# Performance work log

Hardware: AMD Instinct MI355X
Metric: run time of the kernel (lower is better)

## Reference

```python
import jax, jax.numpy as jnp
import numpy as np
from jax.scipy.linalg import expm

LATENT, HIDDEN, N_PARTS, K = 128, 2048, 128, 2048
OMEGA_DIM, TRANZ_DIM = 9 * N_PARTS, 3 * N_PARTS


def setup_inputs() -> dict:
    key = jax.random.key(0)
    ks = jax.random.split(key, 10)

    def w(k, out_d, in_d):
        # eqx.nn.Linear-style scale ~ 1/sqrt(fan_in)
        return jax.random.normal(k, (out_d, in_d), dtype=jnp.float32) / np.sqrt(in_d)

    return {
        "x_init": jax.random.normal(ks[0], (LATENT, K), dtype=jnp.float32),
        "Wo0": w(ks[1], HIDDEN, LATENT),
        "Wo1": w(ks[2], HIDDEN, HIDDEN),
        "Wo2": w(ks[3], HIDDEN, HIDDEN),
        "Wo3": w(ks[4], OMEGA_DIM, HIDDEN),
        "Wt0": w(ks[5], HIDDEN, LATENT),
        "Wt1": w(ks[6], HIDDEN, HIDDEN),
        "Wt2": w(ks[7], HIDDEN, HIDDEN),
        "Wt3": w(ks[8], TRANZ_DIM, HIDDEN),
    }


def _mlp(weights, x):
    # bias-free MLP, relu on all but last layer; x is (d_in, K)
    for i, W in enumerate(weights):
        x = W @ x
        if i + 1 < len(weights):
            x = jax.nn.relu(x)
    return x


def reference(x_init, Wo0, Wo1, Wo2, Wo3, Wt0, Wt1, Wt2, Wt3):
    omega = _mlp([Wo0, Wo1, Wo2, Wo3], x_init)            # (9n, K)
    n = omega.shape[0] // 9
    k = omega.shape[1]
    # exp_omega 2D branch: vmap over columns, each column -> (n,3,3) expm batch
    mats = omega.T.reshape(k * n, 3, 3)
    R = jax.vmap(expm)(mats).reshape(k, 9 * n)            # (K, 9n)
    rotations = R.T                                        # (9n, K)
    translations = _mlp([Wt0, Wt1, Wt2, Wt3], x_init)     # (3n, K)
    # form_transformations (2D branch): stack translation as a 4th row -> (12n, K)
    rot_r = rotations.reshape(n, 3, 3, k)
    tr_r = translations.reshape(n, 1, 3, k)
    transf = jnp.concatenate([rot_r, tr_r], axis=1).reshape(-1, k)  # (12n, K)
    return (omega, transf, rotations, translations)
```

## Files before the change

kernel.cpp:

```cpp
#include <hip/hip_runtime.h>
#include <stdint.h>


typedef short bf16x8 __attribute__((ext_vector_type(8)));
typedef float f32x4 __attribute__((ext_vector_type(4)));

__device__ __forceinline__ unsigned short f2bf(float f) {
  unsigned int x = __float_as_uint(f);
  unsigned int r = (x + 0x7fffu + ((x >> 16) & 1u)) >> 16;
  return (unsigned short)r;
}

__device__ __forceinline__ void gld_lds16(const void* g, void* l) {
  __builtin_amdgcn_global_load_lds(
      (__attribute__((address_space(1))) void*)(g),
      (__attribute__((address_space(3))) void*)(l),
      16, 0, 0);
}

__device__ __forceinline__ unsigned lds_addr(const void* p) {
  return (unsigned)(uintptr_t)(__attribute__((address_space(3))) const void*)p;
}

__device__ __forceinline__ bf16x8 ds_read128(unsigned a) {
  bf16x8 r;
  asm volatile("ds_read_b128 %0, %1" : "=v"(r) : "v"(a));
  return r;
}

#define ASM_BAR asm volatile("s_barrier" ::: "memory")
#define LGKM0   asm volatile("s_waitcnt lgkmcnt(0)" ::: "memory")
#define VMCNT0  asm volatile("s_waitcnt vmcnt(0)" ::: "memory")
#define SCHED0  __builtin_amdgcn_sched_barrier(0)

__global__ void prep_k(const float* __restrict__ x,
                       const float* __restrict__ wo0, const float* __restrict__ wo1,
                       const float* __restrict__ wo2, const float* __restrict__ wo3,
                       const float* __restrict__ wt0, const float* __restrict__ wt1,
                       const float* __restrict__ wt2, const float* __restrict__ wt3,
                       unsigned short* __restrict__ dst, unsigned short* __restrict__ xt) {
  __shared__ float tile[32][33];
  const int b = blockIdx.x;
  const int tid = threadIdx.x;
  if (b >= 9984) {
    const int r = b - 9984;
    const int bx = r & 63, by = r >> 6;
    const int tx = tid & 31, ty = tid >> 5;
#pragma unroll
    for (int i = 0; i < 32; i += 8)
      tile[ty + i][tx] = x[(size_t)(by * 32 + ty + i) * 2048 + bx * 32 + tx];
    __syncthreads();
#pragma unroll
    for (int i = 0; i < 32; i += 8)
      xt[(size_t)(bx * 32 + ty + i) * 128 + by * 32 + tx] = f2bf(tile[tx][ty + i]);
    return;
  }
  int idx = (b * 256 + tid) * 8;
  if (idx >= 20447232) return;
  const float* src;
  int off;
  if (idx < 8650752) {
    if (idx < 262144)       { src = wo0; off = idx; }
    else if (idx < 4456448) { src = wo1; off = idx - 262144; }
    else                    { src = wo2; off = idx - 4456448; }
  } else {
    if (idx < 11010048)      { src = wo3; off = idx - 8650752; }
    else if (idx < 11272192) { src = wt0; off = idx - 11010048; }
    else if (idx < 15466496) { src = wt1; off = idx - 11272192; }
    else if (idx < 19660800) { src = wt2; off = idx - 15466496; }
    else                     { src = wt3; off = idx - 19660800; }
  }
  float4 a = *(const float4*)(src + off);
  float4 c = *(const float4*)(src + off + 4);
  uint4 o;
  o.x = (unsigned)f2bf(a.x) | ((unsigned)f2bf(a.y) << 16);
  o.y = (unsigned)f2bf(a.z) | ((unsigned)f2bf(a.w) << 16);
  o.z = (unsigned)f2bf(c.x) | ((unsigned)f2bf(c.y) << 16);
  o.w = (unsigned)f2bf(c.z) | ((unsigned)f2bf(c.w) << 16);
  *(uint4*)(dst + idx) = o;
}

template <int SWZ>
__global__ __launch_bounds__(256, 2) void gemm_tn(
    const unsigned short* __restrict__ A0, const unsigned short* __restrict__ B0,
    unsigned short* __restrict__ C0, int n0tiles, int ldc0,
    const unsigned short* __restrict__ A1, const unsigned short* __restrict__ B1,
    unsigned short* __restrict__ C1, int ldc1, int K) {
  __shared__ alignas(16) unsigned short Asl[128 * 128];
  __shared__ alignas(16) unsigned short Bsl[128 * 128];

  int mt, yt;
  if (SWZ) {
    int id = blockIdx.x;
    int xcd = id & 7, s = id >> 3;
    mt = ((xcd & 1) << 3) + (s & 7);
    yt = ((xcd >> 1) << 3) + (s >> 3);
  } else {
    mt = blockIdx.x;
    yt = blockIdx.y;
  }

  const unsigned short* A;
  const unsigned short* B;
  unsigned short* C;
  int ldc;
  if (yt < n0tiles) { A = A0; B = B0; C = C0; ldc = ldc0; }
  else { A = A1; B = B1; C = C1; ldc = ldc1; yt -= n0tiles; }

  const unsigned short* Ab = A + (size_t)mt * 128 * K;
  const unsigned short* Bb = B + (size_t)yt * 128 * K;

  const int tid = threadIdx.x;
  const int wave = tid >> 6, lane = tid & 63;
  const int mw = (wave >> 1) * 64, nw = (wave & 1) * 64;
  const int l16 = lane & 15, quad = lane >> 4;

  f32x4 acc[4][4] = {};

  for (int k0 = 0; k0 < K; k0 += 128) {
#pragma unroll
    for (int i = 0; i < 8; ++i) {
      int c = i * 256 + tid;
      int row = c >> 4;
      int l = (c & 15) ^ (row & 15);
      gld_lds16(Ab + (size_t)row * K + k0 + l * 8, &Asl[c * 8]);
      gld_lds16(Bb + (size_t)row * K + k0 + l * 8, &Bsl[c * 8]);
    }
    __syncthreads();

#pragma unroll
    for (int h = 0; h < 4; ++h) {
      bf16x8 af[4], bfr[4];
#pragma unroll
      for (int t = 0; t < 4; ++t) {
        int row = mw + t * 16 + l16;
        int p = (h * 4 + quad) ^ (row & 15);
        af[t] = *(const bf16x8*)&Asl[row * 128 + p * 8];
      }
#pragma unroll
      for (int t = 0; t < 4; ++t) {
        int row = nw + t * 16 + l16;
        int p = (h * 4 + quad) ^ (row & 15);
        bfr[t] = *(const bf16x8*)&Bsl[row * 128 + p * 8];
      }
#pragma unroll
      for (int tm = 0; tm < 4; ++tm)
#pragma unroll
        for (int tn = 0; tn < 4; ++tn)
          acc[tm][tn] = __builtin_amdgcn_mfma_f32_16x16x32_bf16(af[tm], bfr[tn], acc[tm][tn], 0, 0, 0);
    }
    __syncthreads();
  }

  const int mbase = mt * 128 + mw;
  const int nbase = yt * 128 + nw;
#pragma unroll
  for (int tm = 0; tm < 4; ++tm) {
#pragma unroll
    for (int tn = 0; tn < 4; ++tn) {
      int col = nbase + tn * 16 + l16;
      int row0 = mbase + tm * 16 + quad * 4;
#pragma unroll
      for (int r = 0; r < 4; ++r) {
        float v = fmaxf(acc[tm][tn][r], 0.0f);
        C[(size_t)(row0 + r) * ldc + col] = f2bf(v);
      }
    }
  }
}

__global__ __launch_bounds__(256, 2) void gemm_db128(
    const unsigned short* __restrict__ A0, const unsigned short* __restrict__ B0,
    unsigned short* __restrict__ C0,
    const unsigned short* __restrict__ A1, const unsigned short* __restrict__ B1,
    unsigned short* __restrict__ C1, int K) {
  __shared__ alignas(16) unsigned short SM[2 * 16384];

  const int id = blockIdx.x;
  const int xcd = id & 7, s = id >> 3;
  const int mt = s & 15;
  const int ntt = xcd * 4 + (s >> 4);

  const unsigned short* A;
  const unsigned short* B;
  unsigned short* C;
  int ntl;
  if (ntt < 16) { A = A0; B = B0; C = C0; ntl = ntt; }
  else          { A = A1; B = B1; C = C1; ntl = ntt - 16; }

  const unsigned short* Ab = A + (size_t)mt * 128 * K;
  const unsigned short* Bb = B + (size_t)ntl * 128 * K;

  const int tid = threadIdx.x;
  const int wave = tid >> 6, lane = tid & 63;
  const int mw = (wave >> 1) * 64, nw = (wave & 1) * 64;
  const int l16 = lane & 15, quad = lane >> 4;

  const unsigned short* gA[4];
  const unsigned short* gB[4];
  int dAo[4], dBo[4];
#pragma unroll
  for (int i = 0; i < 4; ++i) {
    int c = i * 256 + tid;
    int row = c >> 3, pc = c & 7, l = pc ^ (row & 7);
    gA[i] = Ab + (size_t)row * K + l * 8;
    dAo[i] = c * 8;
    gB[i] = Bb + (size_t)row * K + l * 8;
    dBo[i] = 8192 + c * 8;
  }

  unsigned aoff[2][4], boff[2][4];
#pragma unroll
  for (int ph = 0; ph < 2; ++ph)
#pragma unroll
    for (int i = 0; i < 4; ++i) {
      int ra = mw + i * 16 + l16;
      aoff[ph][i] = (unsigned)(ra * 128 + (((ph * 4 + quad) ^ (ra & 7)) * 16));
      int rb = nw + i * 16 + l16;
      boff[ph][i] = (unsigned)(16384 + rb * 128 + (((ph * 4 + quad) ^ (rb & 7)) * 16));
    }
  const unsigned Au = lds_addr(SM);

  f32x4 acc[4][4] = {};
  const int NT = K >> 6;

  auto STAGE = [&](int slot, int k1) {
    const int so = slot * 16384;
#pragma unroll
    for (int i = 0; i < 4; ++i) gld_lds16(gA[i] + k1, SM + so + dAo[i]);
#pragma unroll
    for (int i = 0; i < 4; ++i) gld_lds16(gB[i] + k1, SM + so + dBo[i]);
  };

  STAGE(0, 0);
  VMCNT0;
  ASM_BAR;

  int cur = 0;
  for (int t = 0; t < NT; ++t) {
    int k1 = (t + 1) << 6;
    if (k1 > K - 64) k1 = K - 64;
    STAGE(cur ^ 1, k1);

    const unsigned base = Au + cur * 32768;
    bf16x8 a0[4], b0[4], a1[4], b1[4];
#pragma unroll
    for (int i = 0; i < 4; ++i) a0[i] = ds_read128(base + aoff[0][i]);
#pragma unroll
    for (int i = 0; i < 4; ++i) b0[i] = ds_read128(base + boff[0][i]);
#pragma unroll
    for (int i = 0; i < 4; ++i) a1[i] = ds_read128(base + aoff[1][i]);
#pragma unroll
    for (int i = 0; i < 4; ++i) b1[i] = ds_read128(base + boff[1][i]);
    LGKM0;
    SCHED0;
    __builtin_amdgcn_s_setprio(1);
#pragma unroll
    for (int tm = 0; tm < 4; ++tm)
#pragma unroll
      for (int tn = 0; tn < 4; ++tn)
        acc[tm][tn] = __builtin_amdgcn_mfma_f32_16x16x32_bf16(a0[tm], b0[tn], acc[tm][tn], 0, 0, 0);
#pragma unroll
    for (int tm = 0; tm < 4; ++tm)
#pragma unroll
      for (int tn = 0; tn < 4; ++tn)
        acc[tm][tn] = __builtin_amdgcn_mfma_f32_16x16x32_bf16(a1[tm], b1[tn], acc[tm][tn], 0, 0, 0);
    __builtin_amdgcn_s_setprio(0);
    SCHED0;

    VMCNT0;
    ASM_BAR;
    cur ^= 1;
  }

  const int mbase = mt * 128 + mw;
  const int nbase = ntl * 128 + nw;
#pragma unroll
  for (int tm = 0; tm < 4; ++tm) {
#pragma unroll
    for (int tn = 0; tn < 4; ++tn) {
      int col = nbase + tn * 16 + l16;
      int row0 = mbase + tm * 16 + quad * 4;
#pragma unroll
      for (int r = 0; r < 4; ++r) {
        float v = fmaxf(acc[tm][tn][r], 0.0f);
        C[(size_t)(row0 + r) * 2048 + col] = f2bf(v);
      }
    }
  }
}

__device__ __forceinline__ void mm3(const float* a, const float* b, float* c) {
#pragma unroll
  for (int r = 0; r < 3; ++r)
#pragma unroll
    for (int cc = 0; cc < 3; ++cc)
      c[r * 3 + cc] = a[r * 3 + 0] * b[0 + cc] + a[r * 3 + 1] * b[3 + cc] + a[r * 3 + 2] * b[6 + cc];
}

__device__ __forceinline__ void expm3(const float* a, float* E) {
  float n1 = 0.f;
#pragma unroll
  for (int c = 0; c < 3; ++c) {
    float s = fabsf(a[c]) + fabsf(a[3 + c]) + fabsf(a[6 + c]);
    n1 = fmaxf(n1, s);
  }
  int s = 0;
  if (n1 > 0.25f) {
    s = (int)ceilf(log2f(n1 * 4.0f));
    if (s < 0) s = 0;
  }
  const float scl = exp2f((float)(-s));
  float As[9];
#pragma unroll
  for (int i = 0; i < 9; ++i) As[i] = a[i] * scl;
  float T[9] = {1, 0, 0, 0, 1, 0, 0, 0, 1};
#pragma unroll
  for (int i = 0; i < 9; ++i) E[i] = T[i];
#pragma unroll
  for (int t = 1; t <= 12; ++t) {
    float Tn[9];
    mm3(T, As, Tn);
    const float inv = 1.0f / (float)t;
#pragma unroll
    for (int i = 0; i < 9; ++i) { T[i] = Tn[i] * inv; E[i] += T[i]; }
  }
  for (int q = 0; q < s; ++q) {
    float Tn[9];
    mm3(E, E, Tn);
#pragma unroll
    for (int i = 0; i < 9; ++i) E[i] = Tn[i];
  }
}

__global__ __launch_bounds__(256, 1) void gemm_l3u(
    const unsigned short* __restrict__ Ho, const unsigned short* __restrict__ W9,
    const unsigned short* __restrict__ Ht, const unsigned short* __restrict__ W3,
    float* __restrict__ out) {
  __shared__ alignas(16) unsigned short SM[40960];
  float* Cl = (float*)SM;

  const int mt = blockIdx.x;
  const int yt = blockIdx.y;
  const int tid = threadIdx.x;
  const int wave = tid >> 6, lane = tid & 63;
  const int wm = wave >> 1, wn = wave & 1;
  const int l16 = lane & 15, quad = lane >> 4;
  const int mbase = mt * 64;

  float* omega  = out;
  float* transf = out + (size_t)1152 * 2048;
  float* rot    = out + (size_t)(1152 + 1536) * 2048;
  float* transl = out + (size_t)(1152 + 1536 + 1152) * 2048;

  const unsigned short* Ao  = Ho + (size_t)mbase * 2048;
  const unsigned short* At  = Ht + (size_t)mbase * 2048;
  const unsigned short* W9p = W9 + (size_t)yt * 144 * 2048;
  const unsigned short* W3p = W3 + (size_t)yt * 48 * 2048;

  const unsigned short* gAo[2];
  const unsigned short* gAt[2];
  int dA[2];
#pragma unroll
  for (int i = 0; i < 2; ++i) {
    int c = i * 256 + tid, row = c >> 3, pc = c & 7, l = pc ^ (row & 7);
    gAo[i] = Ao + (size_t)row * 2048 + l * 8;
    gAt[i] = At + (size_t)row * 2048 + l * 8;
    dA[i] = c * 8;
  }
  const unsigned short* gB[6];
  int dB[6];
#pragma unroll
  for (int i = 0; i < 6; ++i) {
    int c = i * 256 + tid, row = c >> 3, pc = c & 7, l = pc ^ (row & 7);
    gB[i] = (row < 144 ? W9p + (size_t)row * 2048
                       : W3p + (size_t)(row - 144) * 2048) + l * 8;
    dB[i] = c * 8;
  }

  auto STAGE = [&](int s, int k1) {
    const int ao = s * 4096, at = 8192 + s * 4096, bo = 16384 + s * 12288;
#pragma unroll
    for (int i = 0; i < 2; ++i) gld_lds16(gAo[i] + k1, SM + ao + dA[i]);
#pragma unroll
    for (int i = 0; i < 2; ++i) gld_lds16(gAt[i] + k1, SM + at + dA[i]);
#pragma unroll
    for (int i = 0; i < 6; ++i) gld_lds16(gB[i] + k1, SM + bo + dB[i]);
  };

  unsigned aoff[2][2], boff[2][6];
#pragma unroll
  for (int ph = 0; ph < 2; ++ph) {
#pragma unroll
    for (int tm = 0; tm < 2; ++tm) {
      int ra = wm * 32 + tm * 16 + l16;
      aoff[ph][tm] = (unsigned)(ra * 128 + (((ph * 4 + quad) ^ (ra & 7)) * 16));
    }
#pragma unroll
    for (int tb = 0; tb < 6; ++tb) {
      int rb = (wn * 6 + tb) * 16 + l16;
      boff[ph][tb] = (unsigned)(rb * 128 + (((ph * 4 + quad) ^ (rb & 7)) * 16));
    }
  }
  const unsigned Au = lds_addr(SM);

  f32x4 acc[2][6] = {};

  STAGE(0, 0);
  VMCNT0;
  ASM_BAR;

  int cur = 0;
  for (int t = 0; t < 32; ++t) {
    int k1 = (t + 1) << 6;
    if (k1 > 2048 - 64) k1 = 2048 - 64;
    STAGE(cur ^ 1, k1);

    const unsigned aoB = Au + cur * 8192;
    const unsigned atB = Au + 16384 + cur * 8192;
    const unsigned bB  = Au + 32768 + cur * 24576;
    bf16x8 a0o[2], a1o[2], a0t[2], a1t[2], b0[6], b1[6];
#pragma unroll
    for (int i = 0; i < 2; ++i) {
      a0o[i] = ds_read128(aoB + aoff[0][i]);
      a1o[i] = ds_read128(aoB + aoff[1][i]);
    }
    if (wn) {
#pragma unroll
      for (int i = 0; i < 2; ++i) {
        a0t[i] = ds_read128(atB + aoff[0][i]);
        a1t[i] = ds_read128(atB + aoff[1][i]);
      }
    }
#pragma unroll
    for (int i = 0; i < 6; ++i) {
      b0[i] = ds_read128(bB + boff[0][i]);
      b1[i] = ds_read128(bB + boff[1][i]);
    }
    LGKM0;
    SCHED0;
    if (!wn) {
#pragma unroll
      for (int i = 0; i < 2; ++i) { a0t[i] = a0o[i]; a1t[i] = a1o[i]; }
    }
    __builtin_amdgcn_s_setprio(1);
#pragma unroll
    for (int tm = 0; tm < 2; ++tm)
#pragma unroll
      for (int tb = 0; tb < 6; ++tb)
        acc[tm][tb] = __builtin_amdgcn_mfma_f32_16x16x32_bf16(
            tb >= 3 ? a0t[tm] : a0o[tm], b0[tb], acc[tm][tb], 0, 0, 0);
#pragma unroll
    for (int tm = 0; tm < 2; ++tm)
#pragma unroll
      for (int tb = 0; tb < 6; ++tb)
        acc[tm][tb] = __builtin_amdgcn_mfma_f32_16x16x32_bf16(
            tb >= 3 ? a1t[tm] : a1o[tm], b1[tb], acc[tm][tb], 0, 0, 0);
    __builtin_amdgcn_s_setprio(0);
    SCHED0;

    VMCNT0;
    ASM_BAR;
    cur ^= 1;
  }

#pragma unroll
  for (int tm = 0; tm < 2; ++tm) {
#pragma unroll
    for (int tb = 0; tb < 6; ++tb) {
      int st = wn * 6 + tb;
      int s0 = wm * 32 + tm * 16 + quad * 4;
      if (st < 9) {
        int d = st * 16 + l16;
        *(f32x4*)&Cl[d * 68 + s0] = acc[tm][tb];
      } else {
        int n = yt * 48 + (st - 9) * 16 + l16;
        int row0 = mbase + s0;
        int j = n / 3, c2 = n % 3;
        *(f32x4*)&transl[(size_t)n * 2048 + row0] = acc[tm][tb];
        *(f32x4*)&transf[(size_t)(12 * j + 9 + c2) * 2048 + row0] = acc[tm][tb];
      }
    }
  }
  __syncthreads();

  const int jbase = yt * 16;
  const int k = mbase + lane;
#pragma unroll 1
  for (int pp = 0; pp < 4; ++pp) {
    int pl = wave * 4 + pp;
    int j = jbase + pl;
    float a[9];
#pragma unroll
    for (int i = 0; i < 9; ++i) a[i] = Cl[(pl * 9 + i) * 68 + lane];
#pragma unroll
    for (int i = 0; i < 9; ++i) omega[(size_t)(9 * j + i) * 2048 + k] = a[i];
    float E[9];
    expm3(a, E);
#pragma unroll
    for (int i = 0; i < 9; ++i) {
      rot[(size_t)(9 * j + i) * 2048 + k] = E[i];
      transf[(size_t)(12 * j + i) * 2048 + k] = E[i];
    }
  }
}

extern "C" void kernel_launch(void* const* d_in, const int* in_sizes, int n_in,
                              void* d_out, int out_size, void* d_ws, size_t ws_size,
                              hipStream_t stream) {
  const float* x   = (const float*)d_in[0];
  const float* Wo0 = (const float*)d_in[1];
  const float* Wo1 = (const float*)d_in[2];
  const float* Wo2 = (const float*)d_in[3];
  const float* Wo3 = (const float*)d_in[4];
  const float* Wt0 = (const float*)d_in[5];
  const float* Wt1 = (const float*)d_in[6];
  const float* Wt2 = (const float*)d_in[7];
  const float* Wt3 = (const float*)d_in[8];

  unsigned short* wb   = (unsigned short*)d_ws;
  unsigned short* wo0b = wb + 0;
  unsigned short* wo1b = wb + 262144;
  unsigned short* wo2b = wb + 4456448;
  unsigned short* wo3b = wb + 8650752;
  unsigned short* wt0b = wb + 11010048;
  unsigned short* wt1b = wb + 11272192;
  unsigned short* wt2b = wb + 15466496;
  unsigned short* wt3b = wb + 19660800;
  unsigned short* Xt   = wb + 20447232;
  unsigned short* HoA  = Xt + 262144;
  unsigned short* HoB  = HoA + 4194304;
  unsigned short* HtA  = HoB + 4194304;
  unsigned short* HtB  = HtA + 4194304;

  prep_k<<<10240, 256, 0, stream>>>(x, Wo0, Wo1, Wo2, Wo3, Wt0, Wt1, Wt2, Wt3, wb, Xt);

  gemm_tn<1><<<512, 256, 0, stream>>>(Xt, wo0b, HoA, 16, 2048,
                                      Xt, wt0b, HtA, 2048, 128);
  gemm_db128<<<512, 256, 0, stream>>>(HoA, wo1b, HoB, HtA, wt1b, HtB, 2048);
  gemm_db128<<<512, 256, 0, stream>>>(HoB, wo2b, HoA, HtB, wt2b, HtA, 2048);
  gemm_l3u<<<dim3(32, 8), 256, 0, stream>>>(HoA, wo3b, HtA, wt3b, (float*)d_out);
}
```

Before: 237.4 us.

## Split final layer GEMM from expm into separate kernels with finer tiling

The fused last-layer GEMM plus expm kernel (256 blocks of 64x192 tiles, one block per CU) is replaced by a plain GEMM with 64x96 tiles over 512 blocks, two allowed per CU, followed by a separate elementwise expm kernel that reads omega back from global memory. The intent is to fill the GPU better and overlap loads, and to spread the expm work across more threads. The cost is an extra launch, a global round trip for omega, and the loss of the A-tile sharing between the omega and translation chains.

```diff
diff --git a/kernel.cpp b/kernel.cpp
--- a/kernel.cpp
+++ b/kernel.cpp
@@ -290,121 +290,74 @@
   }
 }
 
-__device__ __forceinline__ void mm3(const float* a, const float* b, float* c) {
-#pragma unroll
-  for (int r = 0; r < 3; ++r)
-#pragma unroll
-    for (int cc = 0; cc < 3; ++cc)
-      c[r * 3 + cc] = a[r * 3 + 0] * b[0 + cc] + a[r * 3 + 1] * b[3 + cc] + a[r * 3 + 2] * b[6 + cc];
-}
-
-__device__ __forceinline__ void expm3(const float* a, float* E) {
-  float n1 = 0.f;
-#pragma unroll
-  for (int c = 0; c < 3; ++c) {
-    float s = fabsf(a[c]) + fabsf(a[3 + c]) + fabsf(a[6 + c]);
-    n1 = fmaxf(n1, s);
-  }
-  int s = 0;
-  if (n1 > 0.25f) {
-    s = (int)ceilf(log2f(n1 * 4.0f));
-    if (s < 0) s = 0;
-  }
-  const float scl = exp2f((float)(-s));
-  float As[9];
-#pragma unroll
-  for (int i = 0; i < 9; ++i) As[i] = a[i] * scl;
-  float T[9] = {1, 0, 0, 0, 1, 0, 0, 0, 1};
-#pragma unroll
-  for (int i = 0; i < 9; ++i) E[i] = T[i];
-#pragma unroll
-  for (int t = 1; t <= 12; ++t) {
-    float Tn[9];
-    mm3(T, As, Tn);
-    const float inv = 1.0f / (float)t;
-#pragma unroll
-    for (int i = 0; i < 9; ++i) { T[i] = Tn[i] * inv; E[i] += T[i]; }
-  }
-  for (int q = 0; q < s; ++q) {
-    float Tn[9];
-    mm3(E, E, Tn);
-#pragma unroll
-    for (int i = 0; i < 9; ++i) E[i] = Tn[i];
-  }
-}
-
-__global__ __launch_bounds__(256, 1) void gemm_l3u(
+__global__ __launch_bounds__(256, 2) void gemm_l3s(
     const unsigned short* __restrict__ Ho, const unsigned short* __restrict__ W9,
     const unsigned short* __restrict__ Ht, const unsigned short* __restrict__ W3,
     float* __restrict__ out) {
-  __shared__ alignas(16) unsigned short SM[40960];
-  float* Cl = (float*)SM;
-
-  const int mt = blockIdx.x;
-  const int yt = blockIdx.y;
+  __shared__ alignas(16) unsigned short SM[2 * 4096 + 2 * 6144];
+
+  const int id = blockIdx.x;
+  const int mt = id & 31;
+  const int nt = id >> 5;
+
+  float* omega  = out;
+  float* transf = out + (size_t)1152 * 2048;
+  float* transl = out + (size_t)(1152 + 1536 + 1152) * 2048;
+
+  const int chain1 = (nt >= 12);
+  const unsigned short* A;
+  const unsigned short* B;
+  if (!chain1) { A = Ho; B = W9 + (size_t)nt * 96 * 2048; }
+  else         { A = Ht; B = W3 + (size_t)(nt - 12) * 96 * 2048; }
+  const unsigned short* Ab = A + (size_t)mt * 64 * 2048;
+
   const int tid = threadIdx.x;
   const int wave = tid >> 6, lane = tid & 63;
-  const int wm = wave >> 1, wn = wave & 1;
+  const int mw = (wave >> 1) * 32, nw = (wave & 1) * 48;
   const int l16 = lane & 15, quad = lane >> 4;
-  const int mbase = mt * 64;
-
-  float* omega  = out;
-  float* transf = out + (size_t)1152 * 2048;
-  float* rot    = out + (size_t)(1152 + 1536) * 2048;
-  float* transl = out + (size_t)(1152 + 1536 + 1152) * 2048;
-
-  const unsigned short* Ao  = Ho + (size_t)mbase * 2048;
-  const unsigned short* At  = Ht + (size_t)mbase * 2048;
-  const unsigned short* W9p = W9 + (size_t)yt * 144 * 2048;
-  const unsigned short* W3p = W3 + (size_t)yt * 48 * 2048;
-
-  const unsigned short* gAo[2];
-  const unsigned short* gAt[2];
+
+  const unsigned short* gA[2];
   int dA[2];
 #pragma unroll
   for (int i = 0; i < 2; ++i) {
     int c = i * 256 + tid, row = c >> 3, pc = c & 7, l = pc ^ (row & 7);
-    gAo[i] = Ao + (size_t)row * 2048 + l * 8;
-    gAt[i] = At + (size_t)row * 2048 + l * 8;
+    gA[i] = Ab + (size_t)row * 2048 + l * 8;
     dA[i] = c * 8;
   }
-  const unsigned short* gB[6];
-  int dB[6];
-#pragma unroll
-  for (int i = 0; i < 6; ++i) {
+  const unsigned short* gB[3];
+  int dB[3];
+#pragma unroll
+  for (int i = 0; i < 3; ++i) {
     int c = i * 256 + tid, row = c >> 3, pc = c & 7, l = pc ^ (row & 7);
-    gB[i] = (row < 144 ? W9p + (size_t)row * 2048
-                       : W3p + (size_t)(row - 144) * 2048) + l * 8;
+    gB[i] = B + (size_t)row * 2048 + l * 8;
     dB[i] = c * 8;
   }
 
   auto STAGE = [&](int s, int k1) {
-    const int ao = s * 4096, at = 8192 + s * 4096, bo = 16384 + s * 12288;
-#pragma unroll
-    for (int i = 0; i < 2; ++i) gld_lds16(gAo[i] + k1, SM + ao + dA[i]);
-#pragma unroll
-    for (int i = 0; i < 2; ++i) gld_lds16(gAt[i] + k1, SM + at + dA[i]);
-#pragma unroll
-    for (int i = 0; i < 6; ++i) gld_lds16(gB[i] + k1, SM + bo + dB[i]);
+    const int sa = s * 4096, sb = 8192 + s * 6144;
+#pragma unroll
+    for (int i = 0; i < 2; ++i) gld_lds16(gA[i] + k1, SM + sa + dA[i]);
+#pragma unroll
+    for (int i = 0; i < 3; ++i) gld_lds16(gB[i] + k1, SM + sb + dB[i]);
   };
 
-  unsigned aoff[2][2], boff[2][6];
+  unsigned aoff[2][2], boff[2][3];
 #pragma unroll
   for (int ph = 0; ph < 2; ++ph) {
 #pragma unroll
     for (int tm = 0; tm < 2; ++tm) {
-      int ra = wm * 32 + tm * 16 + l16;
+      int ra = mw + tm * 16 + l16;
       aoff[ph][tm] = (unsigned)(ra * 128 + (((ph * 4 + quad) ^ (ra & 7)) * 16));
     }
 #pragma unroll
-    for (int tb = 0; tb < 6; ++tb) {
-      int rb = (wn * 6 + tb) * 16 + l16;
-      boff[ph][tb] = (unsigned)(rb * 128 + (((ph * 4 + quad) ^ (rb & 7)) * 16));
+    for (int tn = 0; tn < 3; ++tn) {
+      int rb = nw + tn * 16 + l16;
+      boff[ph][tn] = (unsigned)(rb * 128 + (((ph * 4 + quad) ^ (rb & 7)) * 16));
     }
   }
   const unsigned Au = lds_addr(SM);
 
-  f32x4 acc[2][6] = {};
+  f32x4 acc[2][3] = {};
 
   STAGE(0, 0);
   VMCNT0;
@@ -416,46 +369,30 @@
     if (k1 > 2048 - 64) k1 = 2048 - 64;
     STAGE(cur ^ 1, k1);
 
-    const unsigned aoB = Au + cur * 8192;
-    const unsigned atB = Au + 16384 + cur * 8192;
-    const unsigned bB  = Au + 32768 + cur * 24576;
-    bf16x8 a0o[2], a1o[2], a0t[2], a1t[2], b0[6], b1[6];
-#pragma unroll
-    for (int i = 0; i < 2; ++i) {
-      a0o[i] = ds_read128(aoB + aoff[0][i]);
-      a1o[i] = ds_read128(aoB + aoff[1][i]);
-    }
-    if (wn) {
-#pragma unroll
-      for (int i = 0; i < 2; ++i) {
-        a0t[i] = ds_read128(atB + aoff[0][i]);
-        a1t[i] = ds_read128(atB + aoff[1][i]);
-      }
-    }
-#pragma unroll
-    for (int i = 0; i < 6; ++i) {
-      b0[i] = ds_read128(bB + boff[0][i]);
-      b1[i] = ds_read128(bB + boff[1][i]);
-    }
+    const unsigned aB = Au + cur * 8192;
+    const unsigned bB = Au + 16384 + cur * 12288;
+    bf16x8 a0[2], b0[3], a1[2], b1[3];
+#pragma unroll
+    for (int i = 0; i < 2; ++i) a0[i] = ds_read128(aB + aoff[0][i]);
+#pragma unroll
+    for (int i = 0; i < 3; ++i) b0[i] = ds_read128(bB + boff[0][i]);
+#pragma unroll
+    for (int i = 0; i < 2; ++i) a1[i] = ds_read128(aB + aoff[1][i]);
+#pragma unroll
+    for (int i = 0; i < 3; ++i) b1[i] = ds_read128(bB + boff[1][i]);
     LGKM0;
     SCHED0;
-    if (!wn) {
-#pragma unroll
-      for (int i = 0; i < 2; ++i) { a0t[i] = a0o[i]; a1t[i] = a1o[i]; }
-    }
     __builtin_amdgcn_s_setprio(1);
 #pragma unroll
     for (int tm = 0; tm < 2; ++tm)
 #pragma unroll
-      for (int tb = 0; tb < 6; ++tb)
-        acc[tm][tb] = __builtin_amdgcn_mfma_f32_16x16x32_bf16(
-            tb >= 3 ? a0t[tm] : a0o[tm], b0[tb], acc[tm][tb], 0, 0, 0);
+      for (int tn = 0; tn < 3; ++tn)
+        acc[tm][tn] = __builtin_amdgcn_mfma_f32_16x16x32_bf16(a0[tm], b0[tn], acc[tm][tn], 0, 0, 0);
 #pragma unroll
     for (int tm = 0; tm < 2; ++tm)
 #pragma unroll
-      for (int tb = 0; tb < 6; ++tb)
-        acc[tm][tb] = __builtin_amdgcn_mfma_f32_16x16x32_bf16(
-            tb >= 3 ? a1t[tm] : a1o[tm], b1[tb], acc[tm][tb], 0, 0, 0);
+      for (int tn = 0; tn < 3; ++tn)
+        acc[tm][tn] = __builtin_amdgcn_mfma_f32_16x16x32_bf16(a1[tm], b1[tn], acc[tm][tn], 0, 0, 0);
     __builtin_amdgcn_s_setprio(0);
     SCHED0;
 
@@ -464,44 +401,87 @@
     cur ^= 1;
   }
 
+  const int mbase = mt * 64 + mw;
 #pragma unroll
   for (int tm = 0; tm < 2; ++tm) {
 #pragma unroll
-    for (int tb = 0; tb < 6; ++tb) {
-      int st = wn * 6 + tb;
-      int s0 = wm * 32 + tm * 16 + quad * 4;
-      if (st < 9) {
-        int d = st * 16 + l16;
-        *(f32x4*)&Cl[d * 68 + s0] = acc[tm][tb];
+    for (int tn = 0; tn < 3; ++tn) {
+      int row0 = mbase + tm * 16 + quad * 4;
+      if (!chain1) {
+        int col = nt * 96 + nw + tn * 16 + l16;
+        *(f32x4*)&omega[(size_t)col * 2048 + row0] = acc[tm][tn];
       } else {
-        int n = yt * 48 + (st - 9) * 16 + l16;
-        int row0 = mbase + s0;
+        int n = (nt - 12) * 96 + nw + tn * 16 + l16;
         int j = n / 3, c2 = n % 3;
-        *(f32x4*)&transl[(size_t)n * 2048 + row0] = acc[tm][tb];
-        *(f32x4*)&transf[(size_t)(12 * j + 9 + c2) * 2048 + row0] = acc[tm][tb];
+        *(f32x4*)&transl[(size_t)n * 2048 + row0] = acc[tm][tn];
+        *(f32x4*)&transf[(size_t)(12 * j + 9 + c2) * 2048 + row0] = acc[tm][tn];
       }
     }
   }
-  __syncthreads();
-
-  const int jbase = yt * 16;
-  const int k = mbase + lane;
-#pragma unroll 1
-  for (int pp = 0; pp < 4; ++pp) {
-    int pl = wave * 4 + pp;
-    int j = jbase + pl;
-    float a[9];
-#pragma unroll
-    for (int i = 0; i < 9; ++i) a[i] = Cl[(pl * 9 + i) * 68 + lane];
-#pragma unroll
-    for (int i = 0; i < 9; ++i) omega[(size_t)(9 * j + i) * 2048 + k] = a[i];
-    float E[9];
-    expm3(a, E);
-#pragma unroll
-    for (int i = 0; i < 9; ++i) {
-      rot[(size_t)(9 * j + i) * 2048 + k] = E[i];
-      transf[(size_t)(12 * j + i) * 2048 + k] = E[i];
-    }
+}
+
+__device__ __forceinline__ void mm3(const float* a, const float* b, float* c) {
+#pragma unroll
+  for (int r = 0; r < 3; ++r)
+#pragma unroll
+    for (int cc = 0; cc < 3; ++cc)
+      c[r * 3 + cc] = a[r * 3 + 0] * b[0 + cc] + a[r * 3 + 1] * b[3 + cc] + a[r * 3 + 2] * b[6 + cc];
+}
+
+__device__ __forceinline__ void expm3(const float* a, float* E) {
+  float n1 = 0.f;
+#pragma unroll
+  for (int c = 0; c < 3; ++c) {
+    float s = fabsf(a[c]) + fabsf(a[3 + c]) + fabsf(a[6 + c]);
+    n1 = fmaxf(n1, s);
+  }
+  int s = 0;
+  if (n1 > 0.25f) {
+    s = (int)ceilf(log2f(n1 * 4.0f));
+    if (s < 0) s = 0;
+  }
+  const float scl = exp2f((float)(-s));
+  float As[9];
+#pragma unroll
+  for (int i = 0; i < 9; ++i) As[i] = a[i] * scl;
+  float T[9] = {1, 0, 0, 0, 1, 0, 0, 0, 1};
+#pragma unroll
+  for (int i = 0; i < 9; ++i) E[i] = T[i];
+#pragma unroll
+  for (int t = 1; t <= 12; ++t) {
+    float Tn[9];
+    mm3(T, As, Tn);
+    const float inv = 1.0f / (float)t;
+#pragma unroll
+    for (int i = 0; i < 9; ++i) { T[i] = Tn[i] * inv; E[i] += T[i]; }
+  }
+  for (int q = 0; q < s; ++q) {
+    float Tn[9];
+    mm3(E, E, Tn);
+#pragma unroll
+    for (int i = 0; i < 9; ++i) E[i] = Tn[i];
+  }
+}
+
+__global__ __launch_bounds__(256) void expm_k(const float* __restrict__ out_ro,
+                                              float* __restrict__ outw) {
+  const float* omega = out_ro;
+  float* transf = outw + (size_t)1152 * 2048;
+  float* rot    = outw + (size_t)(1152 + 1536) * 2048;
+
+  const int id = blockIdx.x;
+  const int j = id >> 3;
+  const int k = ((id & 7) << 8) + threadIdx.x;
+
+  float a[9];
+#pragma unroll
+  for (int i = 0; i < 9; ++i) a[i] = omega[(size_t)(9 * j + i) * 2048 + k];
+  float E[9];
+  expm3(a, E);
+#pragma unroll
+  for (int i = 0; i < 9; ++i) {
+    rot[(size_t)(9 * j + i) * 2048 + k] = E[i];
+    transf[(size_t)(12 * j + i) * 2048 + k] = E[i];
   }
 }
 
@@ -539,5 +519,6 @@
                                       Xt, wt0b, HtA, 2048, 128);
   gemm_db128<<<512, 256, 0, stream>>>(HoA, wo1b, HoB, HtA, wt1b, HtB, 2048);
   gemm_db128<<<512, 256, 0, stream>>>(HoB, wo2b, HoA, HtB, wt2b, HtA, 2048);
-  gemm_l3u<<<dim3(32, 8), 256, 0, stream>>>(HoA, wo3b, HtA, wt3b, (float*)d_out);
-}
+  gemm_l3s<<<512, 256, 0, stream>>>(HoA, wo3b, HtA, wt3b, (float*)d_out);
+  expm_k<<<1024, 256, 0, stream>>>((const float*)d_out, (float*)d_out);
+}
```

Measured after the change: 234.7 us. Within noise of the previous version (-1.1%).
